# Kernel optimization log

Measured on AMD Instinct MI355X. Metric: run time of the kernel, lower is better.

## Reference

```python
import jax, jax.numpy as jnp
import numpy as np

INPUT_DIM = 8192
HIDDEN = 512
EMBED = HIDDEN // 2  # op embedding dim
NUM_TEMPERS = 64
NUM_OPS = 3
MAX_HOPS = 4
B = 2048


def setup_inputs() -> dict:
    key = jax.random.key(0)
    ks = jax.random.split(key, 10)
    n = lambda k, shape: jax.random.normal(k, shape, jnp.float32)
    return {
        "x": n(ks[0], (B, INPUT_DIM)),
        "op_emb": 0.01 * n(ks[1], (NUM_OPS, EMBED)),
        "op_logits": jnp.zeros((NUM_OPS,), jnp.float32),
        "id_embeds": 0.01 * n(ks[2], (128, 4)),
        "W1": n(ks[3], (HIDDEN + 4 + EMBED, HIDDEN)) / np.sqrt(HIDDEN + 4 + EMBED),
        "b1": jnp.zeros((HIDDEN,), jnp.float32),
        "W2": n(ks[4], (HIDDEN, HIDDEN)) / np.sqrt(HIDDEN),
        "b2": jnp.zeros((HIDDEN,), jnp.float32),
        "Wr1": n(ks[5], (HIDDEN + 4, 32)) / np.sqrt(HIDDEN + 4),
        "br1": jnp.zeros((32,), jnp.float32),
        "Wr2": n(ks[6], (32, NUM_TEMPERS + 1)) / np.sqrt(32),
        "br2": jnp.zeros((NUM_TEMPERS + 1,), jnp.float32),
        "Wp": n(ks[7], (HIDDEN, INPUT_DIM)) / np.sqrt(HIDDEN),
        "bp": jnp.zeros((INPUT_DIM,), jnp.float32),
        "tid_emb": 0.01 * n(ks[8], (NUM_TEMPERS, 4)),
        "rng_seed": 42,
    }


def reference(x, op_emb, op_logits, id_embeds, W1, b1, W2, b2, Wr1, br1, Wr2, br2, Wp, bp, tid_emb, rng_seed):
    Bx, D = x.shape
    # D is a multiple of HIDDEN here -> no padding branch needed
    num_patches = D // HIDDEN
    patch_states = x.reshape(Bx * num_patches, HIDDEN)
    N = patch_states.shape[0]

    rng = jax.random.key(rng_seed)
    rng, tk = jax.random.split(rng)
    patch_tempers = jax.random.randint(tk, (N,), 0, NUM_TEMPERS)
    patch_done = jnp.zeros((N,), bool)

    # Fixed-length unroll of the while_loop (max_hops=4). Early-exit only
    # differs if ALL patches stop early, which is vanishingly unlikely.
    for hop in range(MAX_HOPS):
        # --- gather active patches (inactive slots fill with index 0, as in original) ---
        active_idx = jnp.where(~patch_done, size=N, fill_value=0)[0]
        x_active = patch_states[active_idx]          # [N, HIDDEN]
        t_active = patch_tempers[active_idx]         # [N]
        # --- Temper: sample op per patch, embed, 2-layer relu MLP ---
        rng, ok = jax.random.split(rng)
        op_probs = jax.nn.softmax(op_logits)
        op_idx = jax.random.categorical(ok, jnp.log(op_probs), shape=(N,))
        x_aug = jnp.concatenate([x_active, id_embeds[t_active], op_emb[op_idx]], axis=-1)
        h = jax.nn.relu(x_aug @ W1 + b1)
        h = jax.nn.relu(h @ W2 + b2)                 # [N, HIDDEN]
        # --- scatter back updated states ---
        patch_states = patch_states.at[active_idx].set(h)
        # --- routing policy + categorical sampling of next temper / stop ---
        enriched = jnp.concatenate([h, tid_emb[t_active]], axis=-1)
        logits = jax.nn.relu(enriched @ Wr1 + br1) @ Wr2 + br2
        rng, sk = jax.random.split(rng)
        sampled = jax.random.categorical(sk, jax.nn.log_softmax(logits))
        stop = sampled == NUM_TEMPERS
        next_t = jnp.clip(sampled, 0, NUM_TEMPERS - 1)
        patch_tempers = patch_tempers.at[active_idx].set(next_t)
        patch_done = patch_done.at[active_idx].set(stop)

    latent = patch_states.reshape(Bx, num_patches, HIDDEN).mean(axis=1)  # [B, HIDDEN]
    pred = latent @ Wp + bp                                              # [B, INPUT_DIM]
    return latent, pred
```

## Files before the change

### kernel.cpp

```cpp
#include <hip/hip_runtime.h>
#include <cstdint>
#include <cstddef>


#define NPATCH 32768
#define NHOP 4
#define RSCALE 4096.0f
#define RINV   2.44140625e-4f

typedef unsigned short u16;
typedef __attribute__((ext_vector_type(8))) _Float16 half8;
typedef __attribute__((ext_vector_type(4))) float f32x4;

#define GLDS(gp, lp) __builtin_amdgcn_global_load_lds( \
    (const __attribute__((address_space(1))) void*)(const void*)(gp), \
    (__attribute__((address_space(3))) void*)(void*)(lp), 16, 0, 0)

__device__ __forceinline__ uint32_t rotl32(uint32_t x, int r){ return (x<<r)|(x>>(32-r)); }

__device__ __forceinline__ void tf2x32(uint32_t k0, uint32_t k1, uint32_t x0, uint32_t x1,
                                       uint32_t& o0, uint32_t& o1){
  uint32_t k2 = k0 ^ k1 ^ 0x1BD11BDAu;
  x0 += k0; x1 += k1;
#define TFR(r) { x0 += x1; x1 = rotl32(x1,(r)); x1 ^= x0; }
  TFR(13) TFR(15) TFR(26) TFR(6)   x0 += k1; x1 += k2 + 1u;
  TFR(17) TFR(29) TFR(16) TFR(24)  x0 += k2; x1 += k0 + 2u;
  TFR(13) TFR(15) TFR(26) TFR(6)   x0 += k0; x1 += k1 + 3u;
  TFR(17) TFR(29) TFR(16) TFR(24)  x0 += k1; x1 += k2 + 4u;
  TFR(13) TFR(15) TFR(26) TFR(6)   x0 += k2; x1 += k0 + 5u;
#undef TFR
  o0 = x0; o1 = x1;
}

__device__ __forceinline__ uint32_t jbits32(uint32_t k0, uint32_t k1, uint32_t idx){
  uint32_t a, b; tf2x32(k0, k1, 0u, idx, a, b);
  return a ^ b;
}

__device__ __forceinline__ void jsplit(uint32_t& r0, uint32_t& r1, uint32_t& c0, uint32_t& c1){
  uint32_t n0, n1;
  tf2x32(r0, r1, 0u, 0u, n0, n1);
  tf2x32(r0, r1, 0u, 1u, c0, c1);
  r0 = n0; r1 = n1;
}

__device__ __forceinline__ float jgumbel(uint32_t bits){
  float f = __uint_as_float(0x3f800000u | (bits >> 9)) - 1.0f;
  float u = fmaxf(f, 1.17549435e-38f);
  return -logf(-logf(u));
}

union uhcv { _Float16 h; u16 u; };
__device__ __forceinline__ u16 f2h(float x){ uhcv t; t.h = (_Float16)x; return t.u; }
__device__ __forceinline__ float h2f(u16 b){ uhcv t; t.u = b; return (float)t.h; }
__device__ __forceinline__ void split2s(float v, u16& a0, u16& a1){
  a0 = f2h(v);
  a1 = f2h((v - h2f(a0)) * RSCALE);
}

__global__ void k_keys(const int* __restrict__ seed, const float* __restrict__ op_logits,
                       uint32_t* __restrict__ keys, float* __restrict__ logp3){
  if (threadIdx.x != 0 || blockIdx.x != 0) return;
  uint32_t r0 = 0u, r1 = (uint32_t)seed[0];
  uint32_t c0, c1;
  jsplit(r0, r1, c0, c1); keys[0] = c0; keys[1] = c1;
  for (int h = 0; h < NHOP; h++){
    jsplit(r0, r1, c0, c1); keys[2 + 4*h] = c0; keys[3 + 4*h] = c1;
    jsplit(r0, r1, c0, c1); keys[4 + 4*h] = c0; keys[5 + 4*h] = c1;
  }
  float l0 = op_logits[0], l1 = op_logits[1], l2 = op_logits[2];
  float mm = fmaxf(l0, fmaxf(l1, l2));
  float e0 = expf(l0-mm), e1 = expf(l1-mm), e2 = expf(l2-mm);
  float ssum = e0 + e1 + e2;
  logp3[0] = logf(e0/ssum); logp3[1] = logf(e1/ssum); logp3[2] = logf(e2/ssum);
}

__global__ __launch_bounds__(256)
void k_init(const uint32_t* __restrict__ keys, int* __restrict__ tempers, int* __restrict__ done){
  int i = blockIdx.x*256 + threadIdx.x;
  uint32_t b = jbits32(keys[0], keys[1], (uint32_t)(NPATCH + i));
  tempers[i] = (int)(b & 63u);
  done[i] = 0;
}

__global__ __launch_bounds__(256)
void k_precomp(const float* __restrict__ id_embeds, const float* __restrict__ op_emb,
               const float* __restrict__ tid_emb,
               const float* __restrict__ W1, const float* __restrict__ b1,
               const float* __restrict__ Wr1, const float* __restrict__ br1,
               float* __restrict__ idW, float* __restrict__ opWb, float* __restrict__ tidWb){
  int b = blockIdx.x, tid = threadIdx.x;
  if (b < 64){
    for (int j = tid; j < 512; j += 256){
      float v = 0.f;
      #pragma unroll
      for (int u = 0; u < 4; u++) v = fmaf(id_embeds[b*4+u], W1[(size_t)(512+u)*512 + j], v);
      idW[b*512 + j] = v;
    }
  } else if (b < 67){
    int o = b - 64;
    for (int j = tid; j < 512; j += 256){
      float v = b1[j];
      for (int u = 0; u < 256; u++) v = fmaf(op_emb[o*256+u], W1[(size_t)(516+u)*512 + j], v);
      opWb[o*512 + j] = v;
    }
  } else {
    for (int idx = tid; idx < 2048; idx += 256){
      int t = idx >> 5, c = idx & 31;
      float v = br1[c];
      #pragma unroll
      for (int u = 0; u < 4; u++) v = fmaf(tid_emb[t*4+u], Wr1[(512+u)*32 + c], v);
      tidWb[idx] = v;
    }
  }
}

__global__ __launch_bounds__(256)
void k_splitW(const float* __restrict__ W1, const float* __restrict__ W2,
              const float* __restrict__ Wp, const float* __restrict__ Wr1,
              u16* __restrict__ W1T, u16* __restrict__ W2T, u16* __restrict__ WpT,
              u16* __restrict__ Wr1P){
  __shared__ float t[32][33];
  int blk = blockIdx.x;
  const float* src; u16* dst; int N; int deg; size_t pst; int tb;
  if (blk < 256){ src = W1; dst = W1T; N = 512; deg = 2; pst = (size_t)512*512; tb = blk; }
  else if (blk < 512){ src = W2; dst = W2T; N = 512; deg = 2; pst = (size_t)512*512; tb = blk - 256; }
  else if (blk < 528){ src = Wr1; dst = Wr1P; N = 32; deg = 2; pst = (size_t)32*512; tb = blk - 512; }
  else { src = Wp; dst = WpT; N = 8192; deg = 1; pst = 0; tb = blk - 528; }
  int n0 = (tb >> 4)*32, k0 = (tb & 15)*32;
  if (N == 32){ n0 = 0; k0 = tb*32; }
  int r = threadIdx.x >> 5, c = threadIdx.x & 31;
  for (int rr = r; rr < 32; rr += 8)
    t[rr][c] = src[(size_t)(k0+rr)*N + ((n0 + c) % N)];
  __syncthreads();
  for (int rr = r; rr < 32; rr += 8){
    if (n0 + rr >= N) break;
    float v = t[c][rr];
    size_t o = (size_t)(n0+rr)*512 + k0 + c;
    if (deg == 2){
      u16 a0, a1; split2s(v, a0, a1);
      dst[o] = a0; dst[pst + o] = a1;
    } else {
      dst[o] = f2h(v);
    }
  }
}

__global__ __launch_bounds__(256)
void k_xsplit(const float* __restrict__ x, u16* __restrict__ sP){
  size_t i = ((size_t)blockIdx.x*256 + threadIdx.x)*4;
  float4 v = *(const float4*)(x + i);
  ushort4 p0, p1;
  split2s(v.x, p0.x, p1.x); split2s(v.y, p0.y, p1.y);
  split2s(v.z, p0.z, p1.z); split2s(v.w, p0.w, p1.w);
  const size_t SP = (size_t)NPATCH*512;
  *(ushort4*)(sP + i) = p0; *(ushort4*)(sP + SP + i) = p1;
}

__global__ __launch_bounds__(1024)
void k_scan(const int* __restrict__ done, int* __restrict__ aidx, int* __restrict__ meta){
  __shared__ int cnt[1024];
  int tid = threadIdx.x;
  int base = tid * 32;
  unsigned flags = 0; int c = 0;
  #pragma unroll
  for (int i = 0; i < 32; i++){
    int f = (done[base + i] == 0);
    flags |= ((unsigned)f) << i;
    c += f;
  }
  cnt[tid] = c;
  __syncthreads();
  int val = c;
  for (int off = 1; off < 1024; off <<= 1){
    int v = (tid >= off) ? cnt[tid - off] : 0;
    __syncthreads();
    val += v; cnt[tid] = val;
    __syncthreads();
  }
  int pos = val - c;
  for (int i = 0; i < 32; i++){
    if ((flags >> i) & 1u) aidx[pos++] = base + i;
  }
  __syncthreads();
  int na = cnt[1023];
  for (int j = na + tid; j < NPATCH; j += 1024) aidx[j] = 0;
  if (tid == 0){
    meta[0] = na;
    meta[1] = (na < NPATCH) ? (NPATCH - 1) : 0;
  }
}

__global__ __launch_bounds__(256)
void k_gather(const int* __restrict__ aidx, const int* __restrict__ tempers,
              const uint32_t* __restrict__ keys, const float* __restrict__ logp3,
              int hop, int* __restrict__ t_act, int* __restrict__ op_idx){
  int s = blockIdx.x*256 + threadIdx.x;
  int p = aidx[s];
  t_act[s] = tempers[p];
  uint32_t k0 = keys[2 + 4*hop], k1 = keys[3 + 4*hop];
  float best = 0.f; int bi = 0;
  #pragma unroll
  for (int c = 0; c < 3; c++){
    float v = jgumbel(jbits32(k0, k1, (uint32_t)(3*s + c))) + logp3[c];
    if (c == 0 || v > best){ best = v; bi = c; }
  }
  op_idx[s] = bi;
}

template<int MODE, int DEG>
__global__ __launch_bounds__(256, 2)
void k_mgemm(const u16* __restrict__ Ap, const u16* __restrict__ Bp,
             float* __restrict__ outF, u16* __restrict__ outP,
             const int* __restrict__ aidx, const float* __restrict__ bias,
             const float* __restrict__ idW, const float* __restrict__ opWb,
             const int* __restrict__ t_act, const int* __restrict__ op_idx,
             const int* __restrict__ meta,
             int Ncols, size_t aStride, size_t bStride, size_t oStride){
  __shared__ u16 As[DEG*4096];
  __shared__ u16 Bs[DEG*4096];
  const int tid = threadIdx.x;
  const int L = tid & 63, w = tid >> 6;
  const int m0 = blockIdx.y*128, n0 = blockIdx.x*128;
  const int wr = w >> 1, wc = w & 1;

  const int SPW = DEG*4;
  const bool isA = (w < 2);
  const u16* gB = isA ? Ap : Bp;
  u16* lB = isA ? As : Bs;
  const size_t pstride = isA ? aStride : bStride;
  const u16* gseg[8];
  u16* lseg[8];
  #pragma unroll
  for (int q = 0; q < SPW; q++){
    int ss = (w & 1)*SPW + q;
    int p = ss >> 3, rb = ss & 7;
    int row16 = rb*16 + (L >> 2);
    int grow;
    if (isA) grow = (MODE == 1) ? aidx[m0 + row16] : (m0 + row16);
    else     grow = n0 + row16;
    int swz = (L & 3) ^ ((L >> 2) & 3);
    gseg[q] = gB + p*pstride + (size_t)grow*512 + swz*8;
    lseg[q] = lB + p*4096 + rb*512;
  }

  f32x4 accM[4][4], accR[4][4];
  #pragma unroll
  for (int i = 0; i < 4; i++)
    #pragma unroll
    for (int j = 0; j < 4; j++){ accM[i][j] = (f32x4)0.f; accR[i][j] = (f32x4)0.f; }

  const int rdsw = ((L >> 4) ^ (L & 3))*8;
  const int frow = L & 15;

  for (int kt = 0; kt < 16; kt++){
    __syncthreads();
    #pragma unroll
    for (int q = 0; q < SPW; q++)
      GLDS(gseg[q] + kt*32, lseg[q]);
    __syncthreads();
    #pragma unroll
    for (int pa = 0; pa < DEG; pa++){
      half8 af[4];
      #pragma unroll
      for (int i = 0; i < 4; i++)
        af[i] = *(const half8*)&As[pa*4096 + (wr*64 + i*16 + frow)*32 + rdsw];
      #pragma unroll
      for (int pb = 0; pb < DEG - pa; pb++){
        #pragma unroll
        for (int j = 0; j < 4; j++){
          half8 bf = *(const half8*)&Bs[pb*4096 + (wc*64 + j*16 + frow)*32 + rdsw];
          #pragma unroll
          for (int i = 0; i < 4; i++){
            if (pa + pb == 0)
              accM[i][j] = __builtin_amdgcn_mfma_f32_16x16x32_f16(af[i], bf, accM[i][j], 0, 0, 0);
            else
              accR[i][j] = __builtin_amdgcn_mfma_f32_16x16x32_f16(af[i], bf, accR[i][j], 0, 0, 0);
          }
        }
      }
    }
  }

  const int rbase = m0 + wr*64 + (L >> 4)*4;
  const int cbase = n0 + wc*64 + (L & 15);
  const int w0v = (MODE == 3) ? meta[1] : 0;
  #pragma unroll
  for (int i = 0; i < 4; i++){
    #pragma unroll
    for (int reg = 0; reg < 4; reg++){
      int r = rbase + i*16 + reg;
      if (MODE == 1){
        int t = t_act[r], o = op_idx[r];
        #pragma unroll
        for (int j = 0; j < 4; j++){
          int c = cbase + j*16;
          float v = accM[i][j][reg] + RINV*accR[i][j][reg] + idW[t*512 + c] + opWb[o*512 + c];
          v = fmaxf(v, 0.f);
          u16 a0, a1; split2s(v, a0, a1);
          size_t off = (size_t)r*512 + c;
          outP[off] = a0; outP[oStride + off] = a1;
        }
      } else if (MODE == 3){
        int p = aidx[r];
        bool allowed = (p != 0) || (r == w0v);
        #pragma unroll
        for (int j = 0; j < 4; j++){
          int c = cbase + j*16;
          float v = accM[i][j][reg] + RINV*accR[i][j][reg] + bias[c];
          v = fmaxf(v, 0.f);
          if (allowed){
            u16 a0, a1; split2s(v, a0, a1);
            size_t off = (size_t)p*512 + c;
            outP[off] = a0; outP[oStride + off] = a1;
          }
        }
      } else {
        #pragma unroll
        for (int j = 0; j < 4; j++){
          int c = cbase + j*16;
          float v = accM[i][j][reg] + bias[c];
          if (DEG == 2) v += RINV*accR[i][j][reg];
          outF[(size_t)r*Ncols + c] = v;
        }
      }
    }
  }
}

__global__ __launch_bounds__(256, 2)
void k_routemm(const u16* __restrict__ sP, const u16* __restrict__ Wr1P,
               const int* __restrict__ aidx, const int* __restrict__ t_act,
               const float* __restrict__ tidWb, float* __restrict__ l32g){
  __shared__ u16 As[2*2048];
  __shared__ u16 Bs[2048];
  const int tid = threadIdx.x;
  const int L = tid & 63, w = tid >> 6;
  const int m0 = blockIdx.x*64;
  const size_t SPh = (size_t)NPATCH*512;

  const u16* gseg[2]; u16* lseg[2];
  #pragma unroll
  for (int q = 0; q < 2; q++){
    int ss = w*2 + q;
    int p = ss >> 2, rb = ss & 3;
    int row16 = rb*16 + (L >> 2);
    int grow = aidx[m0 + row16];
    int swz = (L & 3) ^ ((L >> 2) & 3);
    gseg[q] = sP + p*SPh + (size_t)grow*512 + swz*8;
    lseg[q] = As + p*2048 + rb*512;
  }
  const u16* gBp = Wr1P + (size_t)(tid>>7)*16384
                        + (size_t)(((tid>>6)&1)*16 + (tid&15))*512 + ((tid>>4)&3)*8;
  u16* lBp = Bs + w*512;

  f32x4 accM[2], accR[2];
  accM[0] = (f32x4)0.f; accM[1] = (f32x4)0.f;
  accR[0] = (f32x4)0.f; accR[1] = (f32x4)0.f;

  const int rdsw = ((L >> 4) ^ (L & 3))*8;
  for (int kt = 0; kt < 16; kt++){
    __syncthreads();
    #pragma unroll
    for (int q = 0; q < 2; q++)
      GLDS(gseg[q] + kt*32, lseg[q]);
    GLDS(gBp + kt*32, lBp);
    __syncthreads();
    #pragma unroll
    for (int pa = 0; pa < 2; pa++){
      half8 af = *(const half8*)&As[pa*2048 + (w*16 + (L & 15))*32 + rdsw];
      #pragma unroll
      for (int pb = 0; pb < 2 - pa; pb++){
        #pragma unroll
        for (int ct = 0; ct < 2; ct++){
          half8 bf = *(const half8*)&Bs[(pb*2 + ct)*512 + (L >> 4)*128 + (L & 15)*8];
          if (pa + pb == 0)
            accM[ct] = __builtin_amdgcn_mfma_f32_16x16x32_f16(af, bf, accM[ct], 0, 0, 0);
          else
            accR[ct] = __builtin_amdgcn_mfma_f32_16x16x32_f16(af, bf, accR[ct], 0, 0, 0);
        }
      }
    }
  }

  #pragma unroll
  for (int reg = 0; reg < 4; reg++){
    int s = m0 + w*16 + (L >> 4)*4 + reg;
    int t = t_act[s];
    #pragma unroll
    for (int ct = 0; ct < 2; ct++){
      int c = ct*16 + (L & 15);
      float v = accM[ct][reg] + RINV*accR[ct][reg] + tidWb[t*32 + c];
      l32g[(size_t)s*32 + c] = fmaxf(v, 0.f);
    }
  }
}

__global__ __launch_bounds__(256)
void k_sample(const float* __restrict__ l32g, const float* __restrict__ Wr2,
              const float* __restrict__ br2,
              const int* __restrict__ aidx, const int* __restrict__ meta,
              const uint32_t* __restrict__ keys, int hop,
              int* __restrict__ tempers, int* __restrict__ done){
  __shared__ float l32s[8][32];
  const int tid = threadIdx.x;
  const int s0 = blockIdx.x * 8;
  l32s[tid >> 5][tid & 31] = l32g[(size_t)s0*32 + tid];
  __syncthreads();

  const int lane = tid & 63, w = tid >> 6;
  const int half = lane >> 5;
  const uint32_t sk0 = keys[4 + 4*hop], sk1 = keys[5 + 4*hop];
  int smp[2];
  for (int pass = 0; pass < 2; pass++){
    const int psl = w*2 + pass;
    const int ps  = s0 + psl;
    const int c = lane;
    float lg = br2[c];
    #pragma unroll
    for (int k = 0; k < 32; k++) lg = fmaf(l32s[psl][k], Wr2[k*65 + c], lg);
    float lg64 = br2[64];
    #pragma unroll
    for (int k = 0; k < 32; k++) lg64 = fmaf(l32s[psl][k], Wr2[k*65 + 64], lg64);
    float m = lg;
    for (int off = 32; off; off >>= 1) m = fmaxf(m, __shfl_xor(m, off));
    m = fmaxf(m, lg64);
    float se = expf(lg - m);
    for (int off = 32; off; off >>= 1) se += __shfl_xor(se, off);
    se += expf(lg64 - m);
    float Lse = logf(se);
    float g = jgumbel(jbits32(sk0, sk1, (uint32_t)(65*ps + c)));
    float v = (lg - m) - Lse + g;
    int idx = c;
    for (int off = 32; off; off >>= 1){
      float ov = __shfl_xor(v, off);
      int   oi = __shfl_xor(idx, off);
      if (ov > v || (ov == v && oi < idx)){ v = ov; idx = oi; }
    }
    float g64 = jgumbel(jbits32(sk0, sk1, (uint32_t)(65*ps + 64)));
    float v64 = (lg64 - m) - Lse + g64;
    if (v64 > v) idx = 64;
    smp[pass] = idx;
  }

  const int s = s0 + w*2 + half;
  const int mysmp = smp[half];
  const int p = aidx[s];
  const bool allowed = (p != 0) || (s == meta[1]);
  if (allowed && (lane & 31) == 0){
    tempers[p] = (mysmp < 63) ? mysmp : 63;
    done[p]    = (mysmp == 64) ? 1 : 0;
  }
}

__global__ __launch_bounds__(256)
void k_latent2(const u16* __restrict__ sP, float* __restrict__ outF, u16* __restrict__ latP){
  int idx = blockIdx.x*256 + threadIdx.x;
  int b = idx >> 9, j = idx & 511;
  const size_t SP = (size_t)NPATCH*512;
  float s = 0.f;
  #pragma unroll 4
  for (int u = 0; u < 16; u++){
    size_t e = (size_t)(b*16 + u)*512 + j;
    s += h2f(sP[e]) + RINV*h2f(sP[SP + e]);
  }
  s *= 0.0625f;
  outF[idx] = s;
  latP[idx] = f2h(s);
}

template<int MODE>
__global__ __launch_bounds__(256)
void k_gemmF(const float* __restrict__ A, const float* __restrict__ B, float* __restrict__ C,
             int Ncols,
             const int* __restrict__ aidx,
             const float* __restrict__ bias,
             const float* __restrict__ idW, const float* __restrict__ opWb,
             const int* __restrict__ t_act, const int* __restrict__ op_idx){
  __shared__ float As[16][128];
  __shared__ float Bs[16][128];
  const int tid = threadIdx.x;
  const int bx = blockIdx.x, by = blockIdx.y;
  const int tx = tid & 15, ty = tid >> 4;
  const int lr = tid >> 1, lhalf = tid & 1;
  const int srow = by*128 + lr;
  const int arow = (MODE == 1) ? aidx[srow] : srow;
  const float* Ap = A + (size_t)arow*512 + lhalf*8;
  const float* Bp = B + (size_t)(tid >> 4)*Ncols + bx*128 + (tid & 15)*8;

  float acc[8][8];
  #pragma unroll
  for (int i = 0; i < 8; i++)
    #pragma unroll
    for (int j = 0; j < 8; j++) acc[i][j] = 0.f;

  for (int kt = 0; kt < 512; kt += 16){
    float4 a0 = *(const float4*)(Ap + kt);
    float4 a1 = *(const float4*)(Ap + kt + 4);
    float4 g0 = *(const float4*)(Bp + (size_t)kt*Ncols);
    float4 g1 = *(const float4*)(Bp + (size_t)kt*Ncols + 4);
    __syncthreads();
    As[lhalf*8+0][lr] = a0.x; As[lhalf*8+1][lr] = a0.y;
    As[lhalf*8+2][lr] = a0.z; As[lhalf*8+3][lr] = a0.w;
    As[lhalf*8+4][lr] = a1.x; As[lhalf*8+5][lr] = a1.y;
    As[lhalf*8+6][lr] = a1.z; As[lhalf*8+7][lr] = a1.w;
    *(float4*)&Bs[tid>>4][(tid&15)*8]     = g0;
    *(float4*)&Bs[tid>>4][(tid&15)*8 + 4] = g1;
    __syncthreads();
    #pragma unroll
    for (int k = 0; k < 16; k++){
      float4 av0 = *(float4*)&As[k][ty*8];
      float4 av1 = *(float4*)&As[k][ty*8+4];
      float4 bv0 = *(float4*)&Bs[k][tx*4];
      float4 bv1 = *(float4*)&Bs[k][64 + tx*4];
      float av[8] = {av0.x,av0.y,av0.z,av0.w,av1.x,av1.y,av1.z,av1.w};
      float bv[8] = {bv0.x,bv0.y,bv0.z,bv0.w,bv1.x,bv1.y,bv1.z,bv1.w};
      #pragma unroll
      for (int i = 0; i < 8; i++)
        #pragma unroll
        for (int j = 0; j < 8; j++)
          acc[i][j] = fmaf(av[i], bv[j], acc[i][j]);
    }
  }

  const int col0a = bx*128 + tx*4;
  const int col0b = col0a + 64;
  #pragma unroll
  for (int i = 0; i < 8; i++){
    int s = by*128 + ty*8 + i;
    float adda[4], addb[4];
    if (MODE == 1){
      int t = t_act[s], o = op_idx[s];
      float4 ia = *(const float4*)&idW[t*512 + col0a];
      float4 ib = *(const float4*)&idW[t*512 + col0b];
      float4 oa = *(const float4*)&opWb[o*512 + col0a];
      float4 ob = *(const float4*)&opWb[o*512 + col0b];
      adda[0]=ia.x+oa.x; adda[1]=ia.y+oa.y; adda[2]=ia.z+oa.z; adda[3]=ia.w+oa.w;
      addb[0]=ib.x+ob.x; addb[1]=ib.y+ob.y; addb[2]=ib.z+ob.z; addb[3]=ib.w+ob.w;
    } else {
      float4 ba = *(const float4*)&bias[col0a];
      float4 bb = *(const float4*)&bias[col0b];
      adda[0]=ba.x; adda[1]=ba.y; adda[2]=ba.z; adda[3]=ba.w;
      addb[0]=bb.x; addb[1]=bb.y; addb[2]=bb.z; addb[3]=bb.w;
    }
    float4 va, vb;
    float* pa = &va.x; float* pb = &vb.x;
    #pragma unroll
    for (int j = 0; j < 4; j++){
      float v0 = acc[i][j]   + adda[j];
      float v1 = acc[i][j+4] + addb[j];
      if (MODE != 2){ v0 = fmaxf(v0, 0.f); v1 = fmaxf(v1, 0.f); }
      pa[j] = v0; pb[j] = v1;
    }
    *(float4*)(C + (size_t)s*Ncols + col0a) = va;
    *(float4*)(C + (size_t)s*Ncols + col0b) = vb;
  }
}

__global__ __launch_bounds__(256)
void k_routeF(const float* __restrict__ h2, const float* __restrict__ Wr1,
              const float* __restrict__ Wr2, const float* __restrict__ br2,
              const float* __restrict__ tidWb,
              const int* __restrict__ t_act, const int* __restrict__ aidx,
              const int* __restrict__ meta, const uint32_t* __restrict__ keys, int hop,
              float* __restrict__ states, int* __restrict__ tempers, int* __restrict__ done){
  __shared__ float Wr1s[256][32];
  __shared__ float h2s[8][512];
  __shared__ float l32[8][32];

  const int tid = threadIdx.x;
  const int s0 = blockIdx.x * 8;

  for (int i4 = tid; i4 < 8*128; i4 += 256){
    int sl = i4 >> 7, q = i4 & 127;
    *(float4*)&h2s[sl][q*4] = *(const float4*)&h2[(size_t)(s0+sl)*512 + q*4];
  }

  const int lane = tid & 63, w = tid >> 6;
  const int half = lane >> 5, col = lane & 31;
  const int sl = w*2 + half;
  const int s  = s0 + sl;
  const int t  = t_act[s];
  float acc = tidWb[t*32 + col];

  for (int kh = 0; kh < 2; kh++){
    __syncthreads();
    for (int idx = tid; idx < 256*32; idx += 256)
      Wr1s[idx >> 5][idx & 31] = Wr1[kh*8192 + idx];
    __syncthreads();
    const int kb = kh * 256;
    #pragma unroll 4
    for (int k4 = 0; k4 < 64; k4++){
      float4 hv = *(float4*)&h2s[sl][kb + k4*4];
      acc = fmaf(hv.x, Wr1s[k4*4+0][col], acc);
      acc = fmaf(hv.y, Wr1s[k4*4+1][col], acc);
      acc = fmaf(hv.z, Wr1s[k4*4+2][col], acc);
      acc = fmaf(hv.w, Wr1s[k4*4+3][col], acc);
    }
  }
  l32[sl][col] = fmaxf(acc, 0.f);
  __syncthreads();

  const uint32_t sk0 = keys[4 + 4*hop], sk1 = keys[5 + 4*hop];
  int smp[2];
  for (int pass = 0; pass < 2; pass++){
    const int psl = w*2 + pass;
    const int ps  = s0 + psl;
    const int c = lane;
    float lg = br2[c];
    #pragma unroll
    for (int k = 0; k < 32; k++) lg = fmaf(l32[psl][k], Wr2[k*65 + c], lg);
    float lg64 = br2[64];
    #pragma unroll
    for (int k = 0; k < 32; k++) lg64 = fmaf(l32[psl][k], Wr2[k*65 + 64], lg64);
    float m = lg;
    for (int off = 32; off; off >>= 1) m = fmaxf(m, __shfl_xor(m, off));
    m = fmaxf(m, lg64);
    float se = expf(lg - m);
    for (int off = 32; off; off >>= 1) se += __shfl_xor(se, off);
    se += expf(lg64 - m);
    float Lse = logf(se);
    float g = jgumbel(jbits32(sk0, sk1, (uint32_t)(65*ps + c)));
    float v = (lg - m) - Lse + g;
    int idx = c;
    for (int off = 32; off; off >>= 1){
      float ov = __shfl_xor(v, off);
      int   oi = __shfl_xor(idx, off);
      if (ov > v || (ov == v && oi < idx)){ v = ov; idx = oi; }
    }
    float g64 = jgumbel(jbits32(sk0, sk1, (uint32_t)(65*ps + 64)));
    float v64 = (lg64 - m) - Lse + g64;
    if (v64 > v) idx = 64;
    smp[pass] = idx;
  }

  const int mysmp = smp[half];
  const int p = aidx[s];
  const int w0v = meta[1];
  const bool allowed = (p != 0) || (s == w0v);
  if (allowed){
    const float4* src = (const float4*)&h2s[sl][0];
    float4* dst = (float4*)(states + (size_t)p*512);
    for (int q = col; q < 128; q += 32) dst[q] = src[q];
    if (col == 0){
      tempers[p] = (mysmp < 63) ? mysmp : 63;
      done[p]    = (mysmp == 64) ? 1 : 0;
    }
  }
}

__global__ __launch_bounds__(256)
void k_latentF(const float* __restrict__ states, float* __restrict__ out){
  int idx = blockIdx.x*256 + threadIdx.x;
  int b = idx >> 9, j = idx & 511;
  float s = 0.f;
  #pragma unroll
  for (int u = 0; u < 16; u++) s += states[(size_t)(b*16 + u)*512 + j];
  out[idx] = s * 0.0625f;
}

extern "C" void kernel_launch(void* const* d_in, const int* in_sizes, int n_in,
                              void* d_out, int out_size, void* d_ws, size_t ws_size,
                              hipStream_t stream) {
  (void)in_sizes; (void)n_in; (void)out_size;
  const float* x         = (const float*)d_in[0];
  const float* op_emb    = (const float*)d_in[1];
  const float* op_logits = (const float*)d_in[2];
  const float* id_embeds = (const float*)d_in[3];
  const float* W1        = (const float*)d_in[4];
  const float* b1        = (const float*)d_in[5];
  const float* W2        = (const float*)d_in[6];
  const float* b2        = (const float*)d_in[7];
  const float* Wr1       = (const float*)d_in[8];
  const float* br1       = (const float*)d_in[9];
  const float* Wr2       = (const float*)d_in[10];
  const float* br2       = (const float*)d_in[11];
  const float* Wp        = (const float*)d_in[12];
  const float* bp        = (const float*)d_in[13];
  const float* tid_emb   = (const float*)d_in[14];
  const int*   seed      = (const int*)d_in[15];
  float* out = (float*)d_out;

  char* w = (char*)d_ws;
  uint32_t* keys = (uint32_t*)w;
  float* logp3   = (float*)(w + 256);
  int*   meta    = (int*)(w + 512);
  int*   tempers = (int*)(w + 4096);
  int*   done    = tempers + NPATCH;
  int*   t_act   = done + NPATCH;
  int*   op_idx  = t_act + NPATCH;
  int*   aidx    = op_idx + NPATCH;
  float* idW     = (float*)(aidx + NPATCH);
  float* opWb    = idW + 64*512;
  float* tidWb   = opWb + 3*512;

  const size_t SPh = (size_t)NPATCH*512;
  u16* W1T     = (u16*)(w + (1u<<20));
  u16* W2T     = W1T + (size_t)2*512*512;
  u16* Wr1P    = W2T + (size_t)2*512*512;
  u16* WpT     = Wr1P + (size_t)2*32*512;
  u16* latP    = WpT + (size_t)8192*512;
  u16* statesP = latP + (size_t)2048*512;
  u16* h1P     = statesP + 2*SPh;
  float* l32g  = (float*)(h1P + 2*SPh);
  const size_t NEED = (size_t)((char*)(l32g + (size_t)NPATCH*32) - w);

  k_keys<<<1, 64, 0, stream>>>(seed, op_logits, keys, logp3);
  k_init<<<NPATCH/256, 256, 0, stream>>>(keys, tempers, done);
  k_precomp<<<68, 256, 0, stream>>>(id_embeds, op_emb, tid_emb, W1, b1, Wr1, br1,
                                    idW, opWb, tidWb);

  if (ws_size >= NEED){
    k_splitW<<<4624, 256, 0, stream>>>(W1, W2, Wp, Wr1, W1T, W2T, WpT, Wr1P);
    k_xsplit<<<(NPATCH*512/4)/256, 256, 0, stream>>>(x, statesP);

    for (int hop = 0; hop < NHOP; hop++){
      k_scan<<<1, 1024, 0, stream>>>(done, aidx, meta);
      k_gather<<<NPATCH/256, 256, 0, stream>>>(aidx, tempers, keys, logp3, hop, t_act, op_idx);
      k_mgemm<1,2><<<dim3(4, NPATCH/128), 256, 0, stream>>>(
          statesP, W1T, nullptr, h1P, aidx, nullptr, idW, opWb, t_act, op_idx, meta,
          512, SPh, (size_t)512*512, SPh);
      k_mgemm<3,2><<<dim3(4, NPATCH/128), 256, 0, stream>>>(
          h1P, W2T, nullptr, statesP, aidx, b2, nullptr, nullptr, nullptr, nullptr, meta,
          512, SPh, (size_t)512*512, SPh);
      k_routemm<<<NPATCH/64, 256, 0, stream>>>(statesP, Wr1P, aidx, t_act, tidWb, l32g);
      k_sample<<<NPATCH/8, 256, 0, stream>>>(l32g, Wr2, br2, aidx, meta, keys, hop,
                                             tempers, done);
    }

    k_latent2<<<(2048*512)/256, 256, 0, stream>>>(statesP, out, latP);
    k_mgemm<2,1><<<dim3(64, 16), 256, 0, stream>>>(
        latP, WpT, out + 2048*512, nullptr, nullptr, bp, nullptr, nullptr, nullptr, nullptr,
        nullptr, 8192, (size_t)2048*512, (size_t)8192*512, 0);
  } else {
    const size_t BIG0 = 2u<<20;
    const size_t SB   = (size_t)NPATCH * 512 * sizeof(float);
    float *states, *h1, *h2;
    bool copy_states;
    if (ws_size >= BIG0 + 3*SB){
      states = (float*)(w + BIG0);
      h1     = (float*)(w + BIG0 + SB);
      h2     = (float*)(w + BIG0 + 2*SB);
      copy_states = true;
    } else {
      states = (float*)d_in[0];
      h1     = (float*)(w + BIG0);
      h2     = (float*)(w + BIG0 + SB);
      copy_states = false;
    }
    if (copy_states)
      hipMemcpyAsync(states, x, SB, hipMemcpyDeviceToDevice, stream);

    for (int hop = 0; hop < NHOP; hop++){
      k_scan<<<1, 1024, 0, stream>>>(done, aidx, meta);
      k_gather<<<NPATCH/256, 256, 0, stream>>>(aidx, tempers, keys, logp3, hop, t_act, op_idx);
      k_gemmF<1><<<dim3(4, NPATCH/128), 256, 0, stream>>>(states, W1, h1, 512,
                                      aidx, nullptr, idW, opWb, t_act, op_idx);
      k_gemmF<0><<<dim3(4, NPATCH/128), 256, 0, stream>>>(h1, W2, h2, 512,
                                      nullptr, b2, nullptr, nullptr, nullptr, nullptr);
      k_routeF<<<NPATCH/8, 256, 0, stream>>>(h2, Wr1, Wr2, br2, tidWb, t_act, aidx,
                                      meta, keys, hop, states, tempers, done);
    }

    k_latentF<<<(2048*512)/256, 256, 0, stream>>>(states, out);
    k_gemmF<2><<<dim3(8192/128, 2048/128), 256, 0, stream>>>(out, Wp, out + 2048*512, 8192,
                                      nullptr, bp, nullptr, nullptr, nullptr, nullptr);
  }
}
```

Measured before the change: 1.047 ms.

## Double-buffer LDS tiles in GEMM kernels and swizzle workgroup order

Both the main split-precision GEMM and the routing GEMM now use two LDS buffers, issuing global-to-LDS loads for the next K tile before computing on the current one, with explicit vmcnt waits and raw barriers in place of the two __syncthreads per iteration. The main GEMM also remaps workgroup IDs in groups of eight to change the tile order for cache locality, and raises wave priority around the MFMA section. The goal is to hide global load latency behind matrix math. In exchange LDS use doubles (up to 64KB per block when DEG=2), which can cut occupancy, and the hand-written waitcnt logic depends on each wave issuing exactly SPW loads per tile.

```diff
diff --git a/kernel.cpp b/kernel.cpp
--- a/kernel.cpp
+++ b/kernel.cpp
@@ -217,14 +217,21 @@
              const int* __restrict__ t_act, const int* __restrict__ op_idx,
              const int* __restrict__ meta,
              int Ncols, size_t aStride, size_t bStride, size_t oStride){
-  __shared__ u16 As[DEG*4096];
-  __shared__ u16 Bs[DEG*4096];
+  __shared__ u16 As[2*DEG*4096];
+  __shared__ u16 Bs[2*DEG*4096];
   const int tid = threadIdx.x;
   const int L = tid & 63, w = tid >> 6;
-  const int m0 = blockIdx.y*128, n0 = blockIdx.x*128;
+
+  const int gx = (int)gridDim.x;
+  const int nwg = gx * (int)gridDim.y;
+  int lin = (int)blockIdx.y * gx + (int)blockIdx.x;
+  if ((nwg & 7) == 0)
+    lin = (lin & 7) * (nwg >> 3) + (lin >> 3);
+  const int m0 = (lin / gx) * 128, n0 = (lin % gx) * 128;
   const int wr = w >> 1, wc = w & 1;
 
-  const int SPW = DEG*4;
+  constexpr int SPW = DEG*4;
+  constexpr int BUFO = DEG*4096;
   const bool isA = (w < 2);
   const u16* gB = isA ? Ap : Bp;
   u16* lB = isA ? As : Bs;
@@ -253,23 +260,37 @@
   const int rdsw = ((L >> 4) ^ (L & 3))*8;
   const int frow = L & 15;
 
+  #pragma unroll
+  for (int q = 0; q < SPW; q++)
+    GLDS(gseg[q], lseg[q]);
+
+  #pragma unroll 2
   for (int kt = 0; kt < 16; kt++){
-    __syncthreads();
-    #pragma unroll
-    for (int q = 0; q < SPW; q++)
-      GLDS(gseg[q] + kt*32, lseg[q]);
-    __syncthreads();
+    const int cb = (kt & 1) * BUFO;
+    if (kt < 15){
+      const int nb = ((kt + 1) & 1) * BUFO;
+      #pragma unroll
+      for (int q = 0; q < SPW; q++)
+        GLDS(gseg[q] + (kt+1)*32, lseg[q] + nb);
+      asm volatile("s_waitcnt vmcnt(%0)" :: "n"(SPW) : "memory");
+    } else {
+      asm volatile("s_waitcnt vmcnt(0)" ::: "memory");
+    }
+    __builtin_amdgcn_s_barrier();
+    asm volatile("" ::: "memory");
+
+    __builtin_amdgcn_s_setprio(1);
     #pragma unroll
     for (int pa = 0; pa < DEG; pa++){
       half8 af[4];
       #pragma unroll
       for (int i = 0; i < 4; i++)
-        af[i] = *(const half8*)&As[pa*4096 + (wr*64 + i*16 + frow)*32 + rdsw];
+        af[i] = *(const half8*)&As[cb + pa*4096 + (wr*64 + i*16 + frow)*32 + rdsw];
       #pragma unroll
       for (int pb = 0; pb < DEG - pa; pb++){
         #pragma unroll
         for (int j = 0; j < 4; j++){
-          half8 bf = *(const half8*)&Bs[pb*4096 + (wc*64 + j*16 + frow)*32 + rdsw];
+          half8 bf = *(const half8*)&Bs[cb + pb*4096 + (wc*64 + j*16 + frow)*32 + rdsw];
           #pragma unroll
           for (int i = 0; i < 4; i++){
             if (pa + pb == 0)
@@ -280,6 +301,10 @@
         }
       }
     }
+    __builtin_amdgcn_s_setprio(0);
+
+    asm volatile("" ::: "memory");
+    __builtin_amdgcn_s_barrier();
   }
 
   const int rbase = m0 + wr*64 + (L >> 4)*4;
@@ -332,8 +357,8 @@
 void k_routemm(const u16* __restrict__ sP, const u16* __restrict__ Wr1P,
                const int* __restrict__ aidx, const int* __restrict__ t_act,
                const float* __restrict__ tidWb, float* __restrict__ l32g){
-  __shared__ u16 As[2*2048];
-  __shared__ u16 Bs[2048];
+  __shared__ u16 As[2*2*2048];
+  __shared__ u16 Bs[2*2048];
   const int tid = threadIdx.x;
   const int L = tid & 63, w = tid >> 6;
   const int m0 = blockIdx.x*64;
@@ -359,21 +384,37 @@
   accR[0] = (f32x4)0.f; accR[1] = (f32x4)0.f;
 
   const int rdsw = ((L >> 4) ^ (L & 3))*8;
+
+  #pragma unroll
+  for (int q = 0; q < 2; q++) GLDS(gseg[q], lseg[q]);
+  GLDS(gBp, lBp);
+
+  #pragma unroll 2
   for (int kt = 0; kt < 16; kt++){
-    __syncthreads();
-    #pragma unroll
-    for (int q = 0; q < 2; q++)
-      GLDS(gseg[q] + kt*32, lseg[q]);
-    GLDS(gBp + kt*32, lBp);
-    __syncthreads();
+    const int cb  = (kt & 1) * 4096;
+    const int cbB = (kt & 1) * 2048;
+    if (kt < 15){
+      const int nb  = ((kt + 1) & 1) * 4096;
+      const int nbB = ((kt + 1) & 1) * 2048;
+      #pragma unroll
+      for (int q = 0; q < 2; q++)
+        GLDS(gseg[q] + (kt+1)*32, lseg[q] + nb);
+      GLDS(gBp + (kt+1)*32, lBp + nbB);
+      asm volatile("s_waitcnt vmcnt(3)" ::: "memory");
+    } else {
+      asm volatile("s_waitcnt vmcnt(0)" ::: "memory");
+    }
+    __builtin_amdgcn_s_barrier();
+    asm volatile("" ::: "memory");
+
     #pragma unroll
     for (int pa = 0; pa < 2; pa++){
-      half8 af = *(const half8*)&As[pa*2048 + (w*16 + (L & 15))*32 + rdsw];
+      half8 af = *(const half8*)&As[cb + pa*2048 + (w*16 + (L & 15))*32 + rdsw];
       #pragma unroll
       for (int pb = 0; pb < 2 - pa; pb++){
         #pragma unroll
         for (int ct = 0; ct < 2; ct++){
-          half8 bf = *(const half8*)&Bs[(pb*2 + ct)*512 + (L >> 4)*128 + (L & 15)*8];
+          half8 bf = *(const half8*)&Bs[cbB + (pb*2 + ct)*512 + (L >> 4)*128 + (L & 15)*8];
           if (pa + pb == 0)
             accM[ct] = __builtin_amdgcn_mfma_f32_16x16x32_f16(af, bf, accM[ct], 0, 0, 0);
           else
@@ -381,6 +422,9 @@
         }
       }
     }
+
+    asm volatile("" ::: "memory");
+    __builtin_amdgcn_s_barrier();
   }
 
   #pragma unroll
```

New measurement: 994.1 us. 5.1% less time.
